# Kernel tuning notes

Measured on AMD Instinct MI355X. Metric: run time of the kernel, lower is better.

Reference implementation:

```python
import jax, jax.numpy as jnp
import numpy as np

OUT = 56          # roi_align / mask resolution
SCALE = 0.25      # spatial_scale (bases at stride 4)
CO = 14           # raw coefficient resolution


def _roi_align_one(feat, box):
    """torchvision roi_align, aligned=True, sampling_ratio=1.
    feat: [B, H, W] base maps for this roi's image; box: [4] = (x0,y0,x1,y1).
    Returns [B, OUT, OUT]."""
    H, W = feat.shape[1], feat.shape[2]
    s = box * SCALE - 0.5  # aligned=True half-pixel offset
    x0, y0, x1, y1 = s[0], s[1], s[2], s[3]
    bw = (x1 - x0) / OUT
    bh = (y1 - y0) / OUT
    # sampling_ratio=1 -> single sample at each bin center
    xs = x0 + (jnp.arange(OUT, dtype=feat.dtype) + 0.5) * bw
    ys = y0 + (jnp.arange(OUT, dtype=feat.dtype) + 0.5) * bh
    vy = (ys >= -1.0) & (ys <= H)
    vx = (xs >= -1.0) & (xs <= W)
    yc = jnp.clip(ys, 0.0, H - 1)
    xc = jnp.clip(xs, 0.0, W - 1)
    yl = jnp.clip(jnp.floor(yc).astype(jnp.int32), 0, H - 2); yh = yl + 1
    xl = jnp.clip(jnp.floor(xc).astype(jnp.int32), 0, W - 2); xh = xl + 1
    ly = yc - yl; hy = 1.0 - ly
    lx = xc - xl; hx = 1.0 - lx
    fll = feat[:, yl, :][:, :, xl]; flh = feat[:, yl, :][:, :, xh]
    fhl = feat[:, yh, :][:, :, xl]; fhh = feat[:, yh, :][:, :, xh]
    val = (hy[:, None] * (hx[None, :] * fll + lx[None, :] * flh)
           + ly[:, None] * (hx[None, :] * fhl + lx[None, :] * fhh))
    return val * (vy[:, None] & vx[None, :])


def _paste_masks(masks, boxes, img_h, img_w):
    """do_paste_mask: grid_sample(bilinear, align_corners=False, zero pad).
    The grid is separable (y depends on row, x on column), so express it as two
    batched matmuls with tent-kernel weights. masks: [N,56,56] -> [N,img_h,img_w]."""
    x0, y0, x1, y1 = (boxes[:, 0:1], boxes[:, 1:2], boxes[:, 2:3], boxes[:, 3:4])
    gy = ((jnp.arange(img_h, dtype=masks.dtype) + 0.5 - y0) / (y1 - y0)) * 2.0 - 1.0  # [N,H]
    gx = ((jnp.arange(img_w, dtype=masks.dtype) + 0.5 - x0) / (x1 - x0)) * 2.0 - 1.0  # [N,W]
    # unnormalize (align_corners=False): f = (g+1)*size/2 - 0.5
    fy = (gy + 1.0) * OUT * 0.5 - 0.5
    fx = (gx + 1.0) * OUT * 0.5 - 0.5
    idx = jnp.arange(OUT, dtype=masks.dtype)
    Wy = jnp.maximum(0.0, 1.0 - jnp.abs(fy[:, :, None] - idx))  # [N, img_h, 56]
    Wx = jnp.maximum(0.0, 1.0 - jnp.abs(fx[:, :, None] - idx))  # [N, img_w, 56]
    rows = jnp.einsum('nhm,nmw->nhw', Wy, masks)                # [N, img_h, 56]
    return jnp.einsum('nhw,nqw->nhq', rows, Wx)                 # [N, img_h, img_w]


def setup_inputs() -> dict:
    key = jax.random.key(0)
    ks = jax.random.split(key, 6)
    b_h, b_w = 136, 200                 # bases at stride 4 of a 544x800 image
    img_h, img_w = b_h * 4, b_w * 4
    N, Bb = 100, 4
    bases = jax.random.normal(ks[0], (1, Bb, b_h, b_w), jnp.float32)
    x0 = jax.random.uniform(ks[1], (N, 1), minval=0.0, maxval=img_w * 0.55)
    y0 = jax.random.uniform(ks[2], (N, 1), minval=0.0, maxval=img_h * 0.55)
    w = jax.random.uniform(ks[3], (N, 1), minval=32.0, maxval=img_w * 0.4)
    h = jax.random.uniform(ks[4], (N, 1), minval=32.0, maxval=img_h * 0.4)
    boxes = jnp.concatenate([x0, y0,
                             jnp.minimum(x0 + w, img_w - 1.0),
                             jnp.minimum(y0 + h, img_h - 1.0)], axis=1)
    top = jax.random.normal(ks[5], (N, Bb * CO * CO), jnp.float32)
    box_feat = jnp.concatenate([jnp.zeros((N, 1), jnp.float32), boxes, top], axis=1)
    return {"bases": bases, "box_feat": box_feat}


def reference(bases, box_feat):
    bidx = box_feat[:, 0].astype(jnp.int32)
    boxes = box_feat[:, 1:5]
    top_feat = box_feat[:, 5:]
    N = box_feat.shape[0]
    Bb, b_h, b_w = bases.shape[1], bases.shape[2], bases.shape[3]
    # roi_align over all detections
    rois = jax.vmap(lambda i, b: _roi_align_one(bases[i], b))(bidx, boxes)  # [N,B,56,56]
    # merge_bases: upsample 14->56 (bilinear, align_corners=False), softmax over bases, blend
    coeffs = top_feat.reshape(N, Bb, CO, CO)
    coeffs = jax.image.resize(coeffs, (N, Bb, OUT, OUT), method='bilinear')
    coeffs = jax.nn.softmax(coeffs, axis=1)
    masks = jax.nn.sigmoid(jnp.sum(rois * coeffs, axis=1))  # [N,56,56]
    return _paste_masks(masks, boxes, b_h * 4, b_w * 4)      # [N, 4*b_h, 4*b_w]
```

## Files before the change

kernel.cpp:

```cpp
#include <hip/hip_runtime.h>
#include <math.h>

#define OUTD 56
#define COD  14
#define BH   136
#define BW   200
#define IMGH 544
#define IMGW 800
#define BB   4
#define BFS  789
#define RPB  16

__global__ __launch_bounds__(256) void mask_kernel(
    const float* __restrict__ bases,
    const float* __restrict__ box_feat,
    float* __restrict__ masks) {
  const int n = blockIdx.y;
  const int p = blockIdx.x * 256 + threadIdx.x;
  if (p >= OUTD * OUTD) return;
  const int y = p / OUTD;
  const int x = p - y * OUTD;

  const float* bf = box_feat + (size_t)n * BFS;
  const int bidx = (int)bf[0];
  const float x0 = bf[1], y0 = bf[2], x1 = bf[3], y1 = bf[4];
  const float sx0 = x0 * 0.25f - 0.5f;
  const float sy0 = y0 * 0.25f - 0.5f;
  const float bwv = (x1 - x0) * 0.25f * (1.0f / OUTD);
  const float bhv = (y1 - y0) * 0.25f * (1.0f / OUTD);
  const float* feat = bases + (size_t)bidx * BB * BH * BW;
  const float* top  = bf + 5;

  const float ysv = sy0 + ((float)y + 0.5f) * bhv;
  const float xsv = sx0 + ((float)x + 0.5f) * bwv;
  const float valid =
      (ysv >= -1.0f && ysv <= (float)BH && xsv >= -1.0f && xsv <= (float)BW)
          ? 1.0f : 0.0f;
  const float yc = fminf(fmaxf(ysv, 0.0f), (float)(BH - 1));
  const float xc = fminf(fmaxf(xsv, 0.0f), (float)(BW - 1));
  int yl = (int)floorf(yc); yl = yl > (BH - 2) ? (BH - 2) : yl;
  int xl = (int)floorf(xc); xl = xl > (BW - 2) ? (BW - 2) : xl;
  const float ly = yc - (float)yl, hy = 1.0f - ly;
  const float lx = xc - (float)xl, hx = 1.0f - lx;
  const float w00 = hy * hx, w01 = hy * lx, w10 = ly * hx, w11 = ly * lx;

  float cyf = fminf(fmaxf(((float)y + 0.5f) * 0.25f - 0.5f, 0.0f), (float)(COD - 1));
  float cxf = fminf(fmaxf(((float)x + 0.5f) * 0.25f - 0.5f, 0.0f), (float)(COD - 1));
  int cyl = (int)floorf(cyf); cyl = cyl > (COD - 2) ? (COD - 2) : cyl;
  int cxl = (int)floorf(cxf); cxl = cxl > (COD - 2) ? (COD - 2) : cxl;
  const float cly = cyf - (float)cyl, chy = 1.0f - cly;
  const float clx = cxf - (float)cxl, chx = 1.0f - clx;
  const float cw00 = chy * chx, cw01 = chy * clx, cw10 = cly * chx, cw11 = cly * clx;

  float rvals[BB], cvals[BB];
#pragma unroll
  for (int b = 0; b < BB; ++b) {
    const float* fb = feat + b * BH * BW;
    const float r = w00 * fb[yl * BW + xl]       + w01 * fb[yl * BW + xl + 1] +
                    w10 * fb[(yl + 1) * BW + xl] + w11 * fb[(yl + 1) * BW + xl + 1];
    rvals[b] = r * valid;
    const float* tb = top + b * COD * COD;
    cvals[b] = cw00 * tb[cyl * COD + cxl]       + cw01 * tb[cyl * COD + cxl + 1] +
               cw10 * tb[(cyl + 1) * COD + cxl] + cw11 * tb[(cyl + 1) * COD + cxl + 1];
  }

  const float mx = fmaxf(fmaxf(cvals[0], cvals[1]), fmaxf(cvals[2], cvals[3]));
  float e[BB], s = 0.0f;
#pragma unroll
  for (int b = 0; b < BB; ++b) { e[b] = __expf(cvals[b] - mx); s += e[b]; }
  const float inv = 1.0f / s;
  float dot = 0.0f;
#pragma unroll
  for (int b = 0; b < BB; ++b) dot += rvals[b] * (e[b] * inv);
  masks[(size_t)n * (OUTD * OUTD) + p] = 1.0f / (1.0f + __expf(-dot));
}

__global__ __launch_bounds__(256) void paste_kernel(
    const float* __restrict__ masks,
    const float* __restrict__ box_feat,
    float4* __restrict__ out) {
  const int n  = blockIdx.y;
  const int h0 = blockIdx.x * RPB;
  const int tid = threadIdx.x;
  const bool active = tid < (IMGW / 4);

  const float* bf = box_feat + (size_t)n * BFS;
  const float x0 = bf[1], y0 = bf[2], x1 = bf[3], y1 = bf[4];

  const float invw = (float)OUTD / (x1 - x0);
  const float cx = (0.5f - x0) * invw - 0.5f;
  const float invh = (float)OUTD / (y1 - y0);
  const float cy = (0.5f - y0) * invh - 0.5f;

  int   xls[4], xhs[4];
  float wx0[4], wx1[4];
#pragma unroll
  for (int i = 0; i < 4; ++i) {
    const float q  = (float)(tid * 4 + i);
    const float fx = fmaf(q, invw, cx);
    const bool vx = (fx > -1.0f && fx < (float)OUTD);
    const int xl = (int)floorf(fx);
    float w1 = fx - (float)xl;
    float w0 = 1.0f - w1;
    if (xl < 0)            w0 = 0.0f;
    if (xl + 1 > OUTD - 1) w1 = 0.0f;
    int lo = xl     < 0        ? 0        : xl;
    lo     = lo     > OUTD - 1 ? OUTD - 1 : lo;
    int hi = xl + 1 < 0        ? 0        : xl + 1;
    hi     = hi     > OUTD - 1 ? OUTD - 1 : hi;
    xls[i] = lo;
    xhs[i] = hi;
    wx0[i] = vx ? w0 : 0.0f;
    wx1[i] = vx ? w1 : 0.0f;
  }

  const float* mbase = masks + (size_t)n * (OUTD * OUTD);
  float4* orow = out + ((size_t)n * IMGH + h0) * (IMGW / 4) + tid;

  for (int r = 0; r < RPB; ++r) {
    const int h = h0 + r;
    const float fy = fmaf((float)h, invh, cy);
    float4 v = make_float4(0.f, 0.f, 0.f, 0.f);
    if (fy > -1.0f && fy < (float)OUTD) {
      const int ml = (int)floorf(fy);
      float wy1 = fy - (float)ml;
      float wy0 = 1.0f - wy1;
      const int r0 = ml < 0 ? 0 : ml;
      const int r1 = (ml + 1 > OUTD - 1) ? (OUTD - 1) : (ml + 1);
      if (ml < 0)            wy0 = 0.0f;
      if (ml + 1 > OUTD - 1) wy1 = 0.0f;
      const float* m0 = mbase + r0 * OUTD;
      const float* m1 = mbase + r1 * OUTD;
      float res[4];
#pragma unroll
      for (int i = 0; i < 4; ++i) {
        res[i] = wy0 * (wx0[i] * m0[xls[i]] + wx1[i] * m0[xhs[i]]) +
                 wy1 * (wx0[i] * m1[xls[i]] + wx1[i] * m1[xhs[i]]);
      }
      v = make_float4(res[0], res[1], res[2], res[3]);
    }
    if (active) orow[(size_t)r * (IMGW / 4)] = v;
  }
}

extern "C" void kernel_launch(void* const* d_in, const int* in_sizes, int n_in,
                              void* d_out, int out_size, void* d_ws, size_t ws_size,
                              hipStream_t stream) {
  const float* bases    = (const float*)d_in[0];
  const float* box_feat = (const float*)d_in[1];
  const int N = in_sizes[1] / BFS;

  float* masks = (float*)d_ws;

  dim3 g1((OUTD * OUTD + 255) / 256, N);
  mask_kernel<<<g1, 256, 0, stream>>>(bases, box_feat, masks);

  dim3 g2(IMGH / RPB, N);
  paste_kernel<<<g2, 256, 0, stream>>>(masks, box_feat, (float4*)d_out);
}
```

Baseline: 182.6 us.

## Zero-fill output in mask kernel and paste only the box-covered region

```diff
diff --git a/kernel.cpp b/kernel.cpp
--- a/kernel.cpp
+++ b/kernel.cpp
@@ -9,14 +9,28 @@
 #define IMGW 800
 #define BB   4
 #define BFS  789
-#define RPB  16
+#define MCHUNK 13
+#define NFILL  4096
+#define MAXROWS 240
 
-__global__ __launch_bounds__(256) void mask_kernel(
+__global__ __launch_bounds__(256) void mask_fill_kernel(
     const float* __restrict__ bases,
     const float* __restrict__ box_feat,
-    float* __restrict__ masks) {
-  const int n = blockIdx.y;
-  const int p = blockIdx.x * 256 + threadIdx.x;
+    float* __restrict__ masks,
+    float4* __restrict__ out,
+    int maskblk, int total4) {
+  const int b = blockIdx.x;
+
+  if (b >= maskblk) {
+    int i = (b - maskblk) * 256 + (int)threadIdx.x;
+    const int stride = NFILL * 256;
+    const float4 z = make_float4(0.f, 0.f, 0.f, 0.f);
+    for (; i < total4; i += stride) out[i] = z;
+    return;
+  }
+
+  const int n = b / MCHUNK;
+  const int p = (b - n * MCHUNK) * 256 + threadIdx.x;
   if (p >= OUTD * OUTD) return;
   const int y = p / OUTD;
   const int x = p - y * OUTD;
@@ -54,93 +68,90 @@
 
   float rvals[BB], cvals[BB];
 #pragma unroll
-  for (int b = 0; b < BB; ++b) {
-    const float* fb = feat + b * BH * BW;
+  for (int bb = 0; bb < BB; ++bb) {
+    const float* fb = feat + bb * BH * BW;
     const float r = w00 * fb[yl * BW + xl]       + w01 * fb[yl * BW + xl + 1] +
                     w10 * fb[(yl + 1) * BW + xl] + w11 * fb[(yl + 1) * BW + xl + 1];
-    rvals[b] = r * valid;
-    const float* tb = top + b * COD * COD;
-    cvals[b] = cw00 * tb[cyl * COD + cxl]       + cw01 * tb[cyl * COD + cxl + 1] +
-               cw10 * tb[(cyl + 1) * COD + cxl] + cw11 * tb[(cyl + 1) * COD + cxl + 1];
+    rvals[bb] = r * valid;
+    const float* tb = top + bb * COD * COD;
+    cvals[bb] = cw00 * tb[cyl * COD + cxl]       + cw01 * tb[cyl * COD + cxl + 1] +
+                cw10 * tb[(cyl + 1) * COD + cxl] + cw11 * tb[(cyl + 1) * COD + cxl + 1];
   }
 
   const float mx = fmaxf(fmaxf(cvals[0], cvals[1]), fmaxf(cvals[2], cvals[3]));
   float e[BB], s = 0.0f;
 #pragma unroll
-  for (int b = 0; b < BB; ++b) { e[b] = __expf(cvals[b] - mx); s += e[b]; }
+  for (int bb = 0; bb < BB; ++bb) { e[bb] = __expf(cvals[bb] - mx); s += e[bb]; }
   const float inv = 1.0f / s;
   float dot = 0.0f;
 #pragma unroll
-  for (int b = 0; b < BB; ++b) dot += rvals[b] * (e[b] * inv);
+  for (int bb = 0; bb < BB; ++bb) dot += rvals[bb] * (e[bb] * inv);
   masks[(size_t)n * (OUTD * OUTD) + p] = 1.0f / (1.0f + __expf(-dot));
 }
 
-__global__ __launch_bounds__(256) void paste_kernel(
+__global__ __launch_bounds__(128) void paste_kernel(
     const float* __restrict__ masks,
     const float* __restrict__ box_feat,
     float4* __restrict__ out) {
-  const int n  = blockIdx.y;
-  const int h0 = blockIdx.x * RPB;
-  const int tid = threadIdx.x;
-  const bool active = tid < (IMGW / 4);
-
+  const int n = blockIdx.y;
   const float* bf = box_feat + (size_t)n * BFS;
   const float x0 = bf[1], y0 = bf[2], x1 = bf[3], y1 = bf[4];
 
+  const float invh = (float)OUTD / (y1 - y0);
+  const float cy = (0.5f - y0) * invh - 0.5f;
   const float invw = (float)OUTD / (x1 - x0);
   const float cx = (0.5f - x0) * invw - 0.5f;
-  const float invh = (float)OUTD / (y1 - y0);
-  const float cy = (0.5f - y0) * invh - 0.5f;
 
-  int   xls[4], xhs[4];
-  float wx0[4], wx1[4];
+  int h_lo = (int)floorf((-1.0f - cy) / invh) - 1;
+  if (h_lo < 0) h_lo = 0;
+  int h_hi = (int)ceilf(((float)OUTD - cy) / invh) + 2;
+  if (h_hi > IMGH) h_hi = IMGH;
+  const int h = h_lo + blockIdx.x;
+  if (h >= h_hi) return;
+
+  int q_lo = (int)floorf((-1.0f - cx) / invw) - 1;
+  if (q_lo < 0) q_lo = 0;
+  int q_hi = (int)ceilf(((float)OUTD - cx) / invw) + 2;
+  if (q_hi > IMGW) q_hi = IMGW;
+  const int q4_lo = q_lo >> 2;
+  const int q4_hi = (q_hi + 3) >> 2;
+  const int q4 = q4_lo + (int)threadIdx.x;
+  if (q4 >= q4_hi) return;
+
+  const float fy = fmaf((float)h, invh, cy);
+  float4 v = make_float4(0.f, 0.f, 0.f, 0.f);
+  if (fy > -1.0f && fy < (float)OUTD) {
+    const int ml = (int)floorf(fy);
+    float wy1 = fy - (float)ml;
+    float wy0 = 1.0f - wy1;
+    const int r0 = ml < 0 ? 0 : ml;
+    const int r1 = (ml + 1 > OUTD - 1) ? (OUTD - 1) : (ml + 1);
+    if (ml < 0)            wy0 = 0.0f;
+    if (ml + 1 > OUTD - 1) wy1 = 0.0f;
+    const float* m0 = masks + (size_t)n * (OUTD * OUTD) + r0 * OUTD;
+    const float* m1 = masks + (size_t)n * (OUTD * OUTD) + r1 * OUTD;
+    float res[4];
 #pragma unroll
-  for (int i = 0; i < 4; ++i) {
-    const float q  = (float)(tid * 4 + i);
-    const float fx = fmaf(q, invw, cx);
-    const bool vx = (fx > -1.0f && fx < (float)OUTD);
-    const int xl = (int)floorf(fx);
-    float w1 = fx - (float)xl;
-    float w0 = 1.0f - w1;
-    if (xl < 0)            w0 = 0.0f;
-    if (xl + 1 > OUTD - 1) w1 = 0.0f;
-    int lo = xl     < 0        ? 0        : xl;
-    lo     = lo     > OUTD - 1 ? OUTD - 1 : lo;
-    int hi = xl + 1 < 0        ? 0        : xl + 1;
-    hi     = hi     > OUTD - 1 ? OUTD - 1 : hi;
-    xls[i] = lo;
-    xhs[i] = hi;
-    wx0[i] = vx ? w0 : 0.0f;
-    wx1[i] = vx ? w1 : 0.0f;
+    for (int i = 0; i < 4; ++i) {
+      const float q  = (float)(q4 * 4 + i);
+      const float fx = fmaf(q, invw, cx);
+      float r = 0.0f;
+      if (fx > -1.0f && fx < (float)OUTD) {
+        const int xl = (int)floorf(fx);
+        float wx1 = fx - (float)xl;
+        float wx0 = 1.0f - wx1;
+        const int xls = xl < 0 ? 0 : xl;
+        const int xhs = (xl + 1 > OUTD - 1) ? (OUTD - 1) : (xl + 1);
+        if (xl < 0)            wx0 = 0.0f;
+        if (xl + 1 > OUTD - 1) wx1 = 0.0f;
+        r = wy0 * (wx0 * m0[xls] + wx1 * m0[xhs]) +
+            wy1 * (wx0 * m1[xls] + wx1 * m1[xhs]);
+      }
+      res[i] = r;
+    }
+    v = make_float4(res[0], res[1], res[2], res[3]);
   }
-
-  const float* mbase = masks + (size_t)n * (OUTD * OUTD);
-  float4* orow = out + ((size_t)n * IMGH + h0) * (IMGW / 4) + tid;
-
-  for (int r = 0; r < RPB; ++r) {
-    const int h = h0 + r;
-    const float fy = fmaf((float)h, invh, cy);
-    float4 v = make_float4(0.f, 0.f, 0.f, 0.f);
-    if (fy > -1.0f && fy < (float)OUTD) {
-      const int ml = (int)floorf(fy);
-      float wy1 = fy - (float)ml;
-      float wy0 = 1.0f - wy1;
-      const int r0 = ml < 0 ? 0 : ml;
-      const int r1 = (ml + 1 > OUTD - 1) ? (OUTD - 1) : (ml + 1);
-      if (ml < 0)            wy0 = 0.0f;
-      if (ml + 1 > OUTD - 1) wy1 = 0.0f;
-      const float* m0 = mbase + r0 * OUTD;
-      const float* m1 = mbase + r1 * OUTD;
-      float res[4];
-#pragma unroll
-      for (int i = 0; i < 4; ++i) {
-        res[i] = wy0 * (wx0[i] * m0[xls[i]] + wx1[i] * m0[xhs[i]]) +
-                 wy1 * (wx0[i] * m1[xls[i]] + wx1[i] * m1[xhs[i]]);
-      }
-      v = make_float4(res[0], res[1], res[2], res[3]);
-    }
-    if (active) orow[(size_t)r * (IMGW / 4)] = v;
-  }
+  out[((size_t)n * IMGH + h) * (IMGW / 4) + q4] = v;
 }
 
 extern "C" void kernel_launch(void* const* d_in, const int* in_sizes, int n_in,
@@ -151,10 +162,13 @@
   const int N = in_sizes[1] / BFS;
 
   float* masks = (float*)d_ws;
+  const int maskblk = MCHUNK * N;
+  const int total4 = N * IMGH * (IMGW / 4);
 
-  dim3 g1((OUTD * OUTD + 255) / 256, N);
-  mask_kernel<<<g1, 256, 0, stream>>>(bases, box_feat, masks);
+  dim3 g1(maskblk + NFILL);
+  mask_fill_kernel<<<g1, 256, 0, stream>>>(bases, box_feat, masks,
+                                           (float4*)d_out, maskblk, total4);
 
-  dim3 g2(IMGH / RPB, N);
-  paste_kernel<<<g2, 256, 0, stream>>>(masks, box_feat, (float4*)d_out);
+  dim3 g2(MAXROWS, N);
+  paste_kernel<<<g2, 128, 0, stream>>>(masks, box_feat, (float4*)d_out);
 }
```

Result: slower. 186.4 us (+2.1%).

## Fuse mask computation into paste kernel with per-band shared-memory mask rows

Applied to the files above, without the earlier changes.

```diff
diff --git a/kernel.cpp b/kernel.cpp
--- a/kernel.cpp
+++ b/kernel.cpp
@@ -9,137 +9,162 @@
 #define IMGW 800
 #define BB   4
 #define BFS  789
-#define RPB  16
+#define RPB  8
+#define W4   (IMGW / 4)
+#define MAXMR 16
 
-__global__ __launch_bounds__(256) void mask_kernel(
+typedef float f4 __attribute__((ext_vector_type(4)));
+
+__global__ __launch_bounds__(256) void fused_kernel(
     const float* __restrict__ bases,
     const float* __restrict__ box_feat,
-    float* __restrict__ masks) {
-  const int n = blockIdx.y;
-  const int p = blockIdx.x * 256 + threadIdx.x;
-  if (p >= OUTD * OUTD) return;
-  const int y = p / OUTD;
-  const int x = p - y * OUTD;
-
-  const float* bf = box_feat + (size_t)n * BFS;
-  const int bidx = (int)bf[0];
-  const float x0 = bf[1], y0 = bf[2], x1 = bf[3], y1 = bf[4];
-  const float sx0 = x0 * 0.25f - 0.5f;
-  const float sy0 = y0 * 0.25f - 0.5f;
-  const float bwv = (x1 - x0) * 0.25f * (1.0f / OUTD);
-  const float bhv = (y1 - y0) * 0.25f * (1.0f / OUTD);
-  const float* feat = bases + (size_t)bidx * BB * BH * BW;
-  const float* top  = bf + 5;
-
-  const float ysv = sy0 + ((float)y + 0.5f) * bhv;
-  const float xsv = sx0 + ((float)x + 0.5f) * bwv;
-  const float valid =
-      (ysv >= -1.0f && ysv <= (float)BH && xsv >= -1.0f && xsv <= (float)BW)
-          ? 1.0f : 0.0f;
-  const float yc = fminf(fmaxf(ysv, 0.0f), (float)(BH - 1));
-  const float xc = fminf(fmaxf(xsv, 0.0f), (float)(BW - 1));
-  int yl = (int)floorf(yc); yl = yl > (BH - 2) ? (BH - 2) : yl;
-  int xl = (int)floorf(xc); xl = xl > (BW - 2) ? (BW - 2) : xl;
-  const float ly = yc - (float)yl, hy = 1.0f - ly;
-  const float lx = xc - (float)xl, hx = 1.0f - lx;
-  const float w00 = hy * hx, w01 = hy * lx, w10 = ly * hx, w11 = ly * lx;
-
-  float cyf = fminf(fmaxf(((float)y + 0.5f) * 0.25f - 0.5f, 0.0f), (float)(COD - 1));
-  float cxf = fminf(fmaxf(((float)x + 0.5f) * 0.25f - 0.5f, 0.0f), (float)(COD - 1));
-  int cyl = (int)floorf(cyf); cyl = cyl > (COD - 2) ? (COD - 2) : cyl;
-  int cxl = (int)floorf(cxf); cxl = cxl > (COD - 2) ? (COD - 2) : cxl;
-  const float cly = cyf - (float)cyl, chy = 1.0f - cly;
-  const float clx = cxf - (float)cxl, chx = 1.0f - clx;
-  const float cw00 = chy * chx, cw01 = chy * clx, cw10 = cly * chx, cw11 = cly * clx;
-
-  float rvals[BB], cvals[BB];
-#pragma unroll
-  for (int b = 0; b < BB; ++b) {
-    const float* fb = feat + b * BH * BW;
-    const float r = w00 * fb[yl * BW + xl]       + w01 * fb[yl * BW + xl + 1] +
-                    w10 * fb[(yl + 1) * BW + xl] + w11 * fb[(yl + 1) * BW + xl + 1];
-    rvals[b] = r * valid;
-    const float* tb = top + b * COD * COD;
-    cvals[b] = cw00 * tb[cyl * COD + cxl]       + cw01 * tb[cyl * COD + cxl + 1] +
-               cw10 * tb[(cyl + 1) * COD + cxl] + cw11 * tb[(cyl + 1) * COD + cxl + 1];
-  }
-
-  const float mx = fmaxf(fmaxf(cvals[0], cvals[1]), fmaxf(cvals[2], cvals[3]));
-  float e[BB], s = 0.0f;
-#pragma unroll
-  for (int b = 0; b < BB; ++b) { e[b] = __expf(cvals[b] - mx); s += e[b]; }
-  const float inv = 1.0f / s;
-  float dot = 0.0f;
-#pragma unroll
-  for (int b = 0; b < BB; ++b) dot += rvals[b] * (e[b] * inv);
-  masks[(size_t)n * (OUTD * OUTD) + p] = 1.0f / (1.0f + __expf(-dot));
-}
-
-__global__ __launch_bounds__(256) void paste_kernel(
-    const float* __restrict__ masks,
-    const float* __restrict__ box_feat,
-    float4* __restrict__ out) {
+    f4* __restrict__ out) {
   const int n  = blockIdx.y;
   const int h0 = blockIdx.x * RPB;
   const int tid = threadIdx.x;
-  const bool active = tid < (IMGW / 4);
 
   const float* bf = box_feat + (size_t)n * BFS;
-  const float x0 = bf[1], y0 = bf[2], x1 = bf[3], y1 = bf[4];
+  const float x0 = bf[1], y0v = bf[2], x1 = bf[3], y1v = bf[4];
 
+  const float invh = (float)OUTD / (y1v - y0v);
+  const float cyo  = (0.5f - y0v) * invh - 0.5f;
   const float invw = (float)OUTD / (x1 - x0);
-  const float cx = (0.5f - x0) * invw - 0.5f;
-  const float invh = (float)OUTD / (y1 - y0);
-  const float cy = (0.5f - y0) * invh - 0.5f;
+  const float cxo  = (0.5f - x0) * invw - 0.5f;
 
+  const float fy_lo = fmaf((float)h0, invh, cyo);
+  const float fy_hi = fmaf((float)(h0 + RPB - 1), invh, cyo);
+
+  f4* oband = out + ((size_t)n * IMGH + h0) * W4;
+
+  if (!(fy_hi > -1.0f && fy_lo < (float)OUTD)) {
+    const f4 z = (f4)0.0f;
+    for (int i = tid; i < RPB * W4; i += 256)
+      __builtin_nontemporal_store(z, oband + i);
+    return;
+  }
+
+  int rlo = (int)floorf(fy_lo);
+  rlo = rlo < 0 ? 0 : (rlo > OUTD - 1 ? OUTD - 1 : rlo);
+  int rhi = (int)floorf(fy_hi) + 1;
+  rhi = rhi < 0 ? 0 : (rhi > OUTD - 1 ? OUTD - 1 : rhi);
+  const int nrows = rhi - rlo + 1;
+
+  __shared__ float mrows[MAXMR][OUTD];
+
+  {
+    const int bidx = (int)bf[0];
+    const float* feat = bases + (size_t)bidx * BB * BH * BW;
+    const float* top  = bf + 5;
+    const float sx0 = x0 * 0.25f - 0.5f;
+    const float sy0 = y0v * 0.25f - 0.5f;
+    const float bwv = (x1 - x0) * 0.25f * (1.0f / OUTD);
+    const float bhv = (y1v - y0v) * 0.25f * (1.0f / OUTD);
+    const int nev = nrows * OUTD;
+
+    for (int idx = tid; idx < nev; idx += 256) {
+      const int rr = idx / OUTD;
+      const int x  = idx - rr * OUTD;
+      const int y  = rlo + rr;
+
+      const float ysv = sy0 + ((float)y + 0.5f) * bhv;
+      const float xsv = sx0 + ((float)x + 0.5f) * bwv;
+      const float valid =
+          (ysv >= -1.0f && ysv <= (float)BH && xsv >= -1.0f && xsv <= (float)BW)
+              ? 1.0f : 0.0f;
+      const float ycc = fminf(fmaxf(ysv, 0.0f), (float)(BH - 1));
+      const float xcc = fminf(fmaxf(xsv, 0.0f), (float)(BW - 1));
+      int yl = (int)floorf(ycc); yl = yl > (BH - 2) ? (BH - 2) : yl;
+      int xl = (int)floorf(xcc); xl = xl > (BW - 2) ? (BW - 2) : xl;
+      const float ly = ycc - (float)yl, hy = 1.0f - ly;
+      const float lx = xcc - (float)xl, hx = 1.0f - lx;
+      const float w00 = hy * hx, w01 = hy * lx, w10 = ly * hx, w11 = ly * lx;
+
+      float cyf = fminf(fmaxf(((float)y + 0.5f) * 0.25f - 0.5f, 0.0f),
+                        (float)(COD - 1));
+      float cxf = fminf(fmaxf(((float)x + 0.5f) * 0.25f - 0.5f, 0.0f),
+                        (float)(COD - 1));
+      int cyl = (int)floorf(cyf); cyl = cyl > (COD - 2) ? (COD - 2) : cyl;
+      int cxl = (int)floorf(cxf); cxl = cxl > (COD - 2) ? (COD - 2) : cxl;
+      const float cly = cyf - (float)cyl, chy = 1.0f - cly;
+      const float clx = cxf - (float)cxl, chx = 1.0f - clx;
+      const float cw00 = chy * chx, cw01 = chy * clx;
+      const float cw10 = cly * chx, cw11 = cly * clx;
+
+      float rvals[BB], cvals[BB];
+#pragma unroll
+      for (int bb = 0; bb < BB; ++bb) {
+        const float* fb = feat + bb * BH * BW;
+        const float r =
+            w00 * fb[yl * BW + xl]       + w01 * fb[yl * BW + xl + 1] +
+            w10 * fb[(yl + 1) * BW + xl] + w11 * fb[(yl + 1) * BW + xl + 1];
+        rvals[bb] = r * valid;
+        const float* tb = top + bb * COD * COD;
+        cvals[bb] =
+            cw00 * tb[cyl * COD + cxl]       + cw01 * tb[cyl * COD + cxl + 1] +
+            cw10 * tb[(cyl + 1) * COD + cxl] + cw11 * tb[(cyl + 1) * COD + cxl + 1];
+      }
+
+      const float mx = fmaxf(fmaxf(cvals[0], cvals[1]),
+                             fmaxf(cvals[2], cvals[3]));
+      float e[BB], s = 0.0f;
+#pragma unroll
+      for (int bb = 0; bb < BB; ++bb) { e[bb] = __expf(cvals[bb] - mx); s += e[bb]; }
+      const float inv = 1.0f / s;
+      float dot = 0.0f;
+#pragma unroll
+      for (int bb = 0; bb < BB; ++bb) dot += rvals[bb] * (e[bb] * inv);
+      mrows[rr][x] = 1.0f / (1.0f + __expf(-dot));
+    }
+  }
+  __syncthreads();
+
+  const bool active = tid < W4;
   int   xls[4], xhs[4];
   float wx0[4], wx1[4];
 #pragma unroll
   for (int i = 0; i < 4; ++i) {
     const float q  = (float)(tid * 4 + i);
-    const float fx = fmaf(q, invw, cx);
+    const float fx = fmaf(q, invw, cxo);
     const bool vx = (fx > -1.0f && fx < (float)OUTD);
     const int xl = (int)floorf(fx);
     float w1 = fx - (float)xl;
     float w0 = 1.0f - w1;
     if (xl < 0)            w0 = 0.0f;
     if (xl + 1 > OUTD - 1) w1 = 0.0f;
-    int lo = xl     < 0        ? 0        : xl;
-    lo     = lo     > OUTD - 1 ? OUTD - 1 : lo;
-    int hi = xl + 1 < 0        ? 0        : xl + 1;
-    hi     = hi     > OUTD - 1 ? OUTD - 1 : hi;
-    xls[i] = lo;
-    xhs[i] = hi;
+    int lo = xl < 0 ? 0 : xl;
+    lo = lo > OUTD - 1 ? OUTD - 1 : lo;
+    int hi = xl + 1 < 0 ? 0 : xl + 1;
+    hi = hi > OUTD - 1 ? OUTD - 1 : hi;
+    xls[i] = lo; xhs[i] = hi;
     wx0[i] = vx ? w0 : 0.0f;
     wx1[i] = vx ? w1 : 0.0f;
   }
 
-  const float* mbase = masks + (size_t)n * (OUTD * OUTD);
-  float4* orow = out + ((size_t)n * IMGH + h0) * (IMGW / 4) + tid;
-
   for (int r = 0; r < RPB; ++r) {
-    const int h = h0 + r;
-    const float fy = fmaf((float)h, invh, cy);
-    float4 v = make_float4(0.f, 0.f, 0.f, 0.f);
+    const float fy = fmaf((float)(h0 + r), invh, cyo);
+    f4 v = (f4)0.0f;
     if (fy > -1.0f && fy < (float)OUTD) {
       const int ml = (int)floorf(fy);
       float wy1 = fy - (float)ml;
       float wy0 = 1.0f - wy1;
-      const int r0 = ml < 0 ? 0 : ml;
-      const int r1 = (ml + 1 > OUTD - 1) ? (OUTD - 1) : (ml + 1);
       if (ml < 0)            wy0 = 0.0f;
       if (ml + 1 > OUTD - 1) wy1 = 0.0f;
-      const float* m0 = mbase + r0 * OUTD;
-      const float* m1 = mbase + r1 * OUTD;
+      int i0 = ml - rlo;
+      i0 = i0 < 0 ? 0 : (i0 > nrows - 1 ? nrows - 1 : i0);
+      int i1 = ml + 1 - rlo;
+      i1 = i1 < 0 ? 0 : (i1 > nrows - 1 ? nrows - 1 : i1);
+      const float* m0 = mrows[i0];
+      const float* m1 = mrows[i1];
       float res[4];
 #pragma unroll
       for (int i = 0; i < 4; ++i) {
         res[i] = wy0 * (wx0[i] * m0[xls[i]] + wx1[i] * m0[xhs[i]]) +
                  wy1 * (wx0[i] * m1[xls[i]] + wx1[i] * m1[xhs[i]]);
       }
-      v = make_float4(res[0], res[1], res[2], res[3]);
+      v = (f4){res[0], res[1], res[2], res[3]};
     }
-    if (active) orow[(size_t)r * (IMGW / 4)] = v;
+    if (active)
+      __builtin_nontemporal_store(v, oband + (size_t)r * W4 + tid);
   }
 }
 
@@ -150,11 +175,6 @@
   const float* box_feat = (const float*)d_in[1];
   const int N = in_sizes[1] / BFS;
 
-  float* masks = (float*)d_ws;
-
-  dim3 g1((OUTD * OUTD + 255) / 256, N);
-  mask_kernel<<<g1, 256, 0, stream>>>(bases, box_feat, masks);
-
-  dim3 g2(IMGH / RPB, N);
-  paste_kernel<<<g2, 256, 0, stream>>>(masks, box_feat, (float4*)d_out);
+  dim3 g(IMGH / RPB, N);
+  fused_kernel<<<g, 256, 0, stream>>>(bases, box_feat, (f4*)d_out);
 }
```

Result: no change. 182.3 us (-0.2%).
